# Kernel optimization log

Hardware: AMD Instinct MI355X
Metric: run time of the kernel (lower is better)

Reference implementation:

```python
import jax, jax.numpy as jnp
from jax import lax
import numpy as np

L = 2          # num_delimiter_layers
H = 8          # num q/kv heads
MIN_CL = 3
MAX_CL = 16

def rms_norm(x, w, eps=1e-6):
    return x * lax.rsqrt(jnp.mean(x * x, axis=-1, keepdims=True) + eps) * w

def rope(t):
    # t: [B, H, S, Dh], GPT-NeoX style half-split rotation, theta=10000
    Dh, S = t.shape[-1], t.shape[-2]
    half = Dh // 2
    inv = 1.0 / (10000.0 ** (jnp.arange(half, dtype=jnp.float32) / half))
    fr = jnp.arange(S, dtype=jnp.float32)[:, None] * inv  # [S, half]
    cos, sin = jnp.cos(fr), jnp.sin(fr)
    t1, t2 = t[..., :half], t[..., half:]
    return jnp.concatenate([t1 * cos - t2 * sin, t1 * sin + t2 * cos], axis=-1)

def chunk_ids_one(flags):
    # flags: [S] bool (probs > 0.5). Returns per-position chunk id and num chunks.
    S = flags.shape[0]
    # ends take value p+1 for flagged p; fallback to a single end at S-1 if none.
    has_end = jnp.zeros(S + 1, bool).at[1:].set(flags)
    fallback = jnp.zeros(S + 1, bool).at[S - 1].set(True)
    has_end = jnp.where(flags.any(), has_end, fallback)
    idx = jnp.where(has_end, jnp.arange(S + 1), S + 1)  # S+1 = sentinel > any cap
    nxt = lax.associative_scan(jnp.minimum, idx, reverse=True)  # nxt[e] = min end >= e
    def step(carry, t):
        cur_end, cid = carry
        def new(_):
            cap = jnp.minimum(t + MAX_CL, S)
            e = nxt[t + 1]                       # smallest end > t
            e = jnp.where(e <= cap, e, cap)
            e = jnp.where(e - t < MIN_CL, jnp.minimum(t + MIN_CL, S), e)
            return e, cid + 1
        new_end, new_cid = lax.cond(t == cur_end, new, lambda _: (cur_end, cid), None)
        return (new_end, new_cid), new_cid
    (_, last), ids = lax.scan(step, (jnp.int32(0), jnp.int32(-1)), jnp.arange(S, dtype=jnp.int32))
    return ids, last + 1

def _forward(x, ln1, Wq, Wk, Wv, Wo, ln2, W1, W2, head_w, head_b):
    B, S, D = x.shape
    Dh = D // H
    causal = jnp.tril(jnp.ones((S, S), bool))
    scale = 1.0 / np.sqrt(Dh)
    for l in range(L):
        h = rms_norm(x, ln1[l])
        def split_heads(t):
            return t.reshape(B, S, H, Dh).transpose(0, 2, 1, 3)
        q = rope(split_heads(h @ Wq[l]))
        k = rope(split_heads(h @ Wk[l]))
        v = split_heads(h @ Wv[l])
        scores = jnp.einsum('bhqd,bhkd->bhqk', q, k) * scale
        scores = jnp.where(causal, scores, jnp.finfo(scores.dtype).min)
        attn = jax.nn.softmax(scores, axis=-1)
        o = jnp.einsum('bhqk,bhkd->bhqd', attn, v)
        o = o.transpose(0, 2, 1, 3).reshape(B, S, D)
        x = x + o @ Wo[l]
        h = rms_norm(x, ln2[l])
        x = x + jax.nn.gelu(h @ W1[l], approximate=False) @ W2[l]
    logits = (x @ head_w).squeeze(-1) + head_b[0]
    probs = jax.nn.sigmoid(logits)
    chunk_len_loss = jnp.mean(jnp.sum(probs, axis=1))
    return x, probs, chunk_len_loss

def setup_inputs():
    key = jax.random.key(0)
    ks = jax.random.split(key, 10)
    B, S, D = 4, 2048, 512
    F = 4 * D
    sc = 0.02
    return {
        'x': jax.random.normal(ks[0], (B, S, D), jnp.float32),
        'x_ids': jax.random.randint(ks[1], (B, S), 0, 256),
        'ln1': jnp.ones((L, D), jnp.float32),
        'Wq': jax.random.normal(ks[2], (L, D, D), jnp.float32) * sc,
        'Wk': jax.random.normal(ks[3], (L, D, D), jnp.float32) * sc,
        'Wv': jax.random.normal(ks[4], (L, D, D), jnp.float32) * sc,
        'Wo': jax.random.normal(ks[5], (L, D, D), jnp.float32) * sc,
        'ln2': jnp.ones((L, D), jnp.float32),
        'W1': jax.random.normal(ks[6], (L, D, F), jnp.float32) * sc,
        'W2': jax.random.normal(ks[7], (L, F, D), jnp.float32) * sc,
        'head_w': jax.random.normal(ks[8], (D, 1), jnp.float32) * sc,
        'head_b': jnp.zeros((1,), jnp.float32),
    }

def reference(x, x_ids, ln1, Wq, Wk, Wv, Wo, ln2, W1, W2, head_w, head_b):
    B, S, D = x.shape
    x_t, probs, chunk_len_loss = _forward(x, ln1, Wq, Wk, Wv, Wo, ln2, W1, W2, head_w, head_b)
    flags = probs > 0.5
    ids, n_chunks = jax.vmap(chunk_ids_one)(flags)  # ids: [B,S] int32
    # chunks partition [0,S), so block-diagonal mask == chunk-id equality
    attention_masks = ids[:, :, None] == ids[:, None, :]
    # per-batch mean chunk length = S / num_chunks (lengths sum to S)
    avg_chunk_len = jnp.mean(jnp.float32(S) / n_chunks.astype(jnp.float32))
    return (x_t, x_ids, avg_chunk_len, attention_masks, chunk_len_loss)
```

## Files before the change

### kernel.cpp

```cpp
#include <hip/hip_runtime.h>
#include <math.h>

#define S_LEN 2048
#define DMODEL 512
#define NHEAD 8
#define DH 64
#define FDIM 2048

typedef unsigned short ushort_t;
typedef __attribute__((ext_vector_type(8))) short short8_t;
typedef __attribute__((ext_vector_type(4))) float float4_t;

#define MFMA16(a, b, c) __builtin_amdgcn_mfma_f32_16x16x32_bf16(a, b, c, 0, 0, 0)



__device__ __forceinline__ ushort_t f2bf(float x) {
    unsigned u = __float_as_uint(x);
    return (ushort_t)((u + 0x7fffu + ((u >> 16) & 1u)) >> 16);
}
__device__ __forceinline__ float bf2f(ushort_t h) {
    return __uint_as_float((unsigned)h << 16);
}
__device__ __forceinline__ float gelu_f(float x) {
    return 0.5f * x * (1.0f + erff(x * 0.70710678118654752440f));
}
__device__ __forceinline__ void gl_lds16(const void* g, void* l) {
    __builtin_amdgcn_global_load_lds(
        (const __attribute__((address_space(1))) void*)g,
        (__attribute__((address_space(3))) void*)l, 16, 0, 0);
}

__device__ __forceinline__ void stage_tile(const ushort_t* __restrict__ g, int rs,
                                           ushort_t* __restrict__ s, int w, int lane) {
    #pragma unroll
    for (int j = 0; j < 2; ++j) {
        const int c = (w * 2 + j) * 64 + lane;
        const int kk = c >> 8, row = (c >> 2) & 63, q = c & 3;
        const int qs = q ^ ((row >> 1) & 3);
        gl_lds16(g + (size_t)row * rs + kk * 32 + qs * 8, s + c * 8);
    }
}

__global__ void copy_init_k(const float* __restrict__ x, const int* __restrict__ x_ids,
                            float* __restrict__ out) {
    size_t i = (size_t)blockIdx.x * blockDim.x + threadIdx.x;
    float4* o4 = (float4*)out;
    o4[i] = ((const float4*)x)[i];
    if (i < 2048) {
        int4 id4 = ((const int4*)x_ids)[i];
        o4[1048576 + i] = make_float4((float)id4.x, (float)id4.y, (float)id4.z, (float)id4.w);
    }
    if (i == 0) { out[4202496] = 0.0f; out[20979713] = 0.0f; }
}

__global__ __launch_bounds__(256) void rope_tab_k(float2* __restrict__ tab) {
    const int i = blockIdx.x * 256 + threadIdx.x;
    const int s = i >> 5, f = i & 31;
    float inv = powf(10000.0f, -(float)f * (1.0f / 32.0f));
    float sn, cs;
    sincosf((float)s * inv, &sn, &cs);
    tab[i] = make_float2(cs, sn);
}

__global__ __launch_bounds__(256) void tsplit_all_k(const float* __restrict__ Wq,
                                                    const float* __restrict__ Wk,
                                                    const float* __restrict__ Wv,
                                                    const float* __restrict__ Wo,
                                                    const float* __restrict__ W1,
                                                    const float* __restrict__ W2,
                                                    ushort_t* __restrict__ wbuf) {
    __shared__ float T[32][33];
    const int bid = blockIdx.x;
    const int l = bid / 3072;
    const int r = bid % 3072;
    ushort_t* lb = wbuf + (size_t)l * 6291456;
    const float* W; ushort_t* Thi; ushort_t* Tlo; int K, N, ntn, rr;
    if (r < 768) {
        const int which = r >> 8; rr = r & 255;
        W = (which == 0 ? Wq : which == 1 ? Wk : Wv) + (size_t)l * 262144;
        Thi = lb + which * 262144; Tlo = lb + 786432 + which * 262144;
        K = 512; N = 512; ntn = 16;
    } else if (r < 1024) {
        rr = r - 768; W = Wo + (size_t)l * 262144;
        Thi = lb + 1572864; Tlo = lb + 1835008; K = 512; N = 512; ntn = 16;
    } else if (r < 2048) {
        rr = r - 1024; W = W1 + (size_t)l * 1048576;
        Thi = lb + 2097152; Tlo = lb + 3145728; K = 512; N = 2048; ntn = 64;
    } else {
        rr = r - 2048; W = W2 + (size_t)l * 1048576;
        Thi = lb + 4194304; Tlo = lb + 5242880; K = 2048; N = 512; ntn = 16;
    }
    const int n0 = (rr % ntn) * 32, k0 = (rr / ntn) * 32;
    const int tx = threadIdx.x & 31, ty = threadIdx.x >> 5;
    #pragma unroll
    for (int i = 0; i < 4; ++i)
        T[ty + 8 * i][tx] = W[(size_t)(k0 + ty + 8 * i) * N + n0 + tx];
    __syncthreads();
    #pragma unroll
    for (int i = 0; i < 4; ++i) {
        const int n = ty + 8 * i;
        float x = T[tx][n];
        ushort_t hi = f2bf(x);
        Thi[(size_t)(n0 + n) * K + k0 + tx] = hi;
        Tlo[(size_t)(n0 + n) * K + k0 + tx] = f2bf(x - bf2f(hi));
    }
}

__global__ __launch_bounds__(256) void rmsnorm_split_k(const float* __restrict__ x,
                                                       const float* __restrict__ w,
                                                       ushort_t* __restrict__ hhi,
                                                       ushort_t* __restrict__ hlo) {
    __shared__ float red[4];
    const int tid = threadIdx.x;
    const size_t row = blockIdx.x;
    const float* xr = x + row * DMODEL;
    float2 v = *(const float2*)(xr + tid * 2);
    float ss = v.x * v.x + v.y * v.y;
    #pragma unroll
    for (int off = 32; off; off >>= 1) ss += __shfl_down(ss, off);
    if ((tid & 63) == 0) red[tid >> 6] = ss;
    __syncthreads();
    float tot = red[0] + red[1] + red[2] + red[3];
    float rs = 1.0f / sqrtf(tot * (1.0f / 512.0f) + 1e-6f);
    float2 wv = *(const float2*)(w + tid * 2);
    float y0 = v.x * rs * wv.x, y1 = v.y * rs * wv.y;
    ushort_t h0 = f2bf(y0), h1 = f2bf(y1);
    ushort_t l0 = f2bf(y0 - bf2f(h0)), l1 = f2bf(y1 - bf2f(h1));
    *(unsigned*)(hhi + row * DMODEL + tid * 2) = ((unsigned)h1 << 16) | h0;
    *(unsigned*)(hlo + row * DMODEL + tid * 2) = ((unsigned)l1 << 16) | l0;
}

template<int EPI, int TN>
__global__ __launch_bounds__(256) void gemm_s(const ushort_t* __restrict__ Ahi,
                                              const ushort_t* __restrict__ Alo,
                                              const ushort_t* __restrict__ Bhi,
                                              const ushort_t* __restrict__ Blo,
                                              int K, int N,
                                              float* __restrict__ C,
                                              const float* __restrict__ Cin,
                                              ushort_t* __restrict__ Chi,
                                              ushort_t* __restrict__ Clo,
                                              ushort_t* __restrict__ oqh,
                                              ushort_t* __restrict__ oql,
                                              ushort_t* __restrict__ okh,
                                              ushort_t* __restrict__ okl,
                                              ushort_t* __restrict__ ovh,
                                              const float2* __restrict__ rtab) {
    constexpr int MT = (TN == 128) ? 4 : 2;
    __shared__ ushort_t sAhi[4096], sAlo[4096];
    __shared__ ushort_t sBhi[TN * 32], sBlo[TN * 32];
    const int tid = threadIdx.x;
    const int lane = tid & 63, w = tid >> 6;
    const int wm = (TN == 128) ? (w >> 1) : w;
    const int wn = (TN == 128) ? (w & 1) : 0;
    const int bm = blockIdx.y, bn = blockIdx.x;
    const int sm = lane >> 2;
    const int sk = ((lane & 3) ^ ((sm >> 1) & 3)) * 8;
    const int fr = lane & 15;
    const int fq = lane >> 4;
    const int fko = (fq ^ ((fr >> 1) & 3)) * 8;

    float4_t acc[MT][4] = {};

    for (int kt = 0; kt < K; kt += 32) {
        #pragma unroll
        for (int j = 0; j < 2; ++j) {
            const int chunk = w * 2 + j;
            const int mr = chunk * 16 + sm;
            const size_t ga = (size_t)(bm * 128 + mr) * K + kt + sk;
            gl_lds16(Ahi + ga, &sAhi[chunk * 512]);
            gl_lds16(Alo + ga, &sAlo[chunk * 512]);
        }
        #pragma unroll
        for (int j = 0; j < TN / 64; ++j) {
            const int chunk = w * (TN / 64) + j;
            const int mr = chunk * 16 + sm;
            const size_t gb = (size_t)(bn * TN + mr) * K + kt + sk;
            gl_lds16(Bhi + gb, &sBhi[chunk * 512]);
            gl_lds16(Blo + gb, &sBlo[chunk * 512]);
        }
        __syncthreads();
        short8_t ah[MT], al[MT], bh[4], bl[4];
        #pragma unroll
        for (int t = 0; t < MT; ++t) {
            const int ao = (wm * (MT * 16) + t * 16 + fr) * 32 + fko;
            ah[t] = *(const short8_t*)&sAhi[ao];
            al[t] = *(const short8_t*)&sAlo[ao];
        }
        #pragma unroll
        for (int t = 0; t < 4; ++t) {
            const int bo = (wn * 64 + t * 16 + fr) * 32 + fko;
            bh[t] = *(const short8_t*)&sBhi[bo];
            bl[t] = *(const short8_t*)&sBlo[bo];
        }
        #pragma unroll
        for (int tm = 0; tm < MT; ++tm)
            #pragma unroll
            for (int tn = 0; tn < 4; ++tn) {
                acc[tm][tn] = MFMA16(ah[tm], bh[tn], acc[tm][tn]);
                acc[tm][tn] = MFMA16(al[tm], bh[tn], acc[tm][tn]);
                acc[tm][tn] = MFMA16(ah[tm], bl[tn], acc[tm][tn]);
            }
        __syncthreads();
    }

    if (EPI == 0) {
        const int cb = bn * 128 + wn * 64;
        const int mat = cb >> 9;
        const int hh = (cb >> 6) & 7;
        #pragma unroll
        for (int tm = 0; tm < MT; ++tm) {
            #pragma unroll
            for (int r = 0; r < 4; ++r) {
                const int mg = bm * 128 + wm * (MT * 16) + tm * 16 + fq * 4 + r;
                const int b = mg >> 11, s = mg & 2047;
                const int bhh = b * NHEAD + hh;
                if (mat < 2) {
                    ushort_t* dhi = (mat == 0) ? oqh : okh;
                    ushort_t* dlo = (mat == 0) ? oql : okl;
                    const size_t base = ((size_t)bhh * S_LEN + s) * DH;
                    #pragma unroll
                    for (int tn = 0; tn < 2; ++tn) {
                        const int d1 = tn * 16 + fr;
                        const float v1 = acc[tm][tn][r], v2 = acc[tm][tn + 2][r];
                        const float2 t = rtab[s * 32 + d1];
                        float r1 = v1 * t.x - v2 * t.y;
                        float r2 = v1 * t.y + v2 * t.x;
                        if (mat == 0) { r1 *= 0.125f; r2 *= 0.125f; }
                        ushort_t h1 = f2bf(r1), h2 = f2bf(r2);
                        dhi[base + d1]      = h1;
                        dlo[base + d1]      = f2bf(r1 - bf2f(h1));
                        dhi[base + d1 + 32] = h2;
                        dlo[base + d1 + 32] = f2bf(r2 - bf2f(h2));
                    }
                } else {
                    #pragma unroll
                    for (int tn = 0; tn < 4; ++tn) {
                        const int d = tn * 16 + fr;
                        const size_t off = ((size_t)bhh * DH + d) * S_LEN + s;
                        ovh[off] = f2bf(acc[tm][tn][r]);
                    }
                }
            }
        }
    } else {
        #pragma unroll
        for (int tm = 0; tm < MT; ++tm) {
            #pragma unroll
            for (int tn = 0; tn < 4; ++tn) {
                const int cb = bn * TN + wn * 64 + tn * 16;
                #pragma unroll
                for (int r = 0; r < 4; ++r) {
                    const int mg = bm * 128 + wm * (MT * 16) + tm * 16 + fq * 4 + r;
                    const float val = acc[tm][tn][r];
                    const size_t off = (size_t)mg * N + cb + fr;
                    if (EPI == 1) {
                        C[off] = Cin[off] + val;
                    } else {
                        const float g = gelu_f(val);
                        const ushort_t hi = f2bf(g);
                        Chi[off] = hi;
                        Clo[off] = f2bf(g - bf2f(hi));
                    }
                }
            }
        }
    }
}

__global__ __launch_bounds__(256) void attn_k(const ushort_t* __restrict__ qhi,
                                              const ushort_t* __restrict__ qlo,
                                              const ushort_t* __restrict__ khi,
                                              const ushort_t* __restrict__ klo,
                                              const ushort_t* __restrict__ vthi,
                                              ushort_t* __restrict__ Ohi,
                                              ushort_t* __restrict__ Olo) {
    __shared__ __align__(16) ushort_t sKh[4096], sKl[4096];
    __shared__ __align__(16) ushort_t sVh[4096], sPh[4096];
    const int tid = threadIdx.x, lane = tid & 63, w = tid >> 6;
    const int fr = lane & 15, fq = lane >> 4;
    const int fko = (fq ^ ((fr >> 1) & 3)) * 8;
    const int bidx = blockIdx.x;
    const int bh = bidx & 31;
    const int qt = 31 - (bidx >> 5);

    short8_t qfh[2], qfl[2];
    {
        const size_t base = ((size_t)bh * S_LEN + qt * 64 + w * 16 + fr) * DH + fq * 8;
        qfh[0] = *(const short8_t*)(qhi + base);
        qfh[1] = *(const short8_t*)(qhi + base + 32);
        qfl[0] = *(const short8_t*)(qlo + base);
        qfl[1] = *(const short8_t*)(qlo + base + 32);
    }

    float m_r[4], l_r[4];
    float4_t oacc[4] = {};
    #pragma unroll
    for (int r = 0; r < 4; ++r) { m_r[r] = -INFINITY; l_r[r] = 0.0f; }

    auto step = [&](const int kt, const bool diag) {
        __syncthreads();
        const size_t ko = ((size_t)bh * S_LEN + kt * 64) * DH;
        stage_tile(khi + ko, 64, sKh, w, lane);
        stage_tile(klo + ko, 64, sKl, w, lane);
        const size_t vo = (size_t)bh * DH * S_LEN + kt * 64;
        stage_tile(vthi + vo, S_LEN, sVh, w, lane);
        __syncthreads();

        float4_t sacc[4] = {};
        #pragma unroll
        for (int kk = 0; kk < 2; ++kk) {
            #pragma unroll
            for (int n = 0; n < 4; ++n) {
                const int bb = kk * 2048 + (n * 16 + fr) * 32 + fko;
                short8_t kh2 = *(const short8_t*)&sKh[bb];
                short8_t kl2 = *(const short8_t*)&sKl[bb];
                sacc[n] = MFMA16(qfh[kk], kh2, sacc[n]);
                sacc[n] = MFMA16(qfl[kk], kh2, sacc[n]);
                sacc[n] = MFMA16(qfh[kk], kl2, sacc[n]);
            }
        }

        #pragma unroll
        for (int r = 0; r < 4; ++r) {
            const int rowl = fq * 4 + r;
            const int qrow = w * 16 + rowl;
            const int psw = (qrow >> 1) & 3;
            float sv[4], mx = -INFINITY;
            #pragma unroll
            for (int n = 0; n < 4; ++n) {
                float x = sacc[n][r];
                if (diag && (n * 16 + fr) > qrow - w * 16 + w * 16) {}
                sv[n] = x;
            }
            #pragma unroll
            for (int n = 0; n < 4; ++n) {
                if (diag && (n * 16 + fr) > qrow) sv[n] = -1e30f;
                mx = fmaxf(mx, sv[n]);
            }
            mx = fmaxf(mx, __shfl_xor(mx, 1));
            mx = fmaxf(mx, __shfl_xor(mx, 2));
            mx = fmaxf(mx, __shfl_xor(mx, 4));
            mx = fmaxf(mx, __shfl_xor(mx, 8));
            const float mn = fmaxf(m_r[r], mx);
            const float alp = __expf(m_r[r] - mn);
            m_r[r] = mn;
            float ls = 0.0f;
            #pragma unroll
            for (int n = 0; n < 4; ++n) {
                const float p = __expf(sv[n] - mn);
                const int c0 = (n & 1) * 16 + fr;
                const int idx = (n >> 1) * 2048 + qrow * 32 + ((c0 >> 3) ^ psw) * 8 + (c0 & 7);
                sPh[idx] = f2bf(p);
                ls += p;
            }
            ls += __shfl_xor(ls, 1);
            ls += __shfl_xor(ls, 2);
            ls += __shfl_xor(ls, 4);
            ls += __shfl_xor(ls, 8);
            l_r[r] = alp * l_r[r] + ls;
            #pragma unroll
            for (int n = 0; n < 4; ++n) oacc[n][r] *= alp;
        }

        #pragma unroll
        for (int kkj = 0; kkj < 2; ++kkj) {
            short8_t ph = *(const short8_t*)&sPh[kkj * 2048 + (w * 16 + fr) * 32 + fko];
            #pragma unroll
            for (int n = 0; n < 4; ++n) {
                short8_t vh = *(const short8_t*)&sVh[kkj * 2048 + (n * 16 + fr) * 32 + fko];
                oacc[n] = MFMA16(ph, vh, oacc[n]);
            }
        }
    };

    for (int kt = 0; kt < qt; ++kt) step(kt, false);
    step(qt, true);

    const int b = bh >> 3, hh = bh & 7;
    #pragma unroll
    for (int r = 0; r < 4; ++r) {
        const float inv_l = 1.0f / l_r[r];
        const int s = qt * 64 + w * 16 + fq * 4 + r;
        const size_t base = ((size_t)b * S_LEN + s) * DMODEL + hh * DH;
        #pragma unroll
        for (int n = 0; n < 4; ++n) {
            const float y = oacc[n][r] * inv_l;
            const ushort_t h = f2bf(y);
            Ohi[base + n * 16 + fr] = h;
            Olo[base + n * 16 + fr] = f2bf(y - bf2f(h));
        }
    }
}

__global__ __launch_bounds__(256) void head_k(const float* __restrict__ x,
                                              const float* __restrict__ w,
                                              const float* __restrict__ b,
                                              float* __restrict__ probs) {
    const int tid = threadIdx.x;
    const int lane = tid & 63;
    const size_t row = (size_t)blockIdx.x * 4 + (tid >> 6);
    const float* xr = x + row * DMODEL;
    float acc = 0.0f;
    #pragma unroll
    for (int i = 0; i < 8; ++i) acc += xr[lane + i * 64] * w[lane + i * 64];
    #pragma unroll
    for (int off = 32; off; off >>= 1) acc += __shfl_down(acc, off);
    if (lane == 0)
        probs[row] = 1.0f / (1.0f + expf(-(acc + b[0])));
}

__global__ __launch_bounds__(256) void chunk_k(const float* __restrict__ probs,
                                               int* __restrict__ ids,
                                               float* __restrict__ avg_out,
                                               float* __restrict__ loss_out) {
    __shared__ ushort_t nxA[2052], nxB[2052];
    __shared__ ushort_t lift[10][2052];
    __shared__ float lred[4];
    __shared__ int anyf;
    const int b = blockIdx.x, tid = threadIdx.x;
    const float* pr = probs + (size_t)b * S_LEN;
    if (tid == 0) anyf = 0;
    __syncthreads();
    int loc = 0;
    float lsum = 0.0f;
    for (int t = tid; t < S_LEN; t += 256) {
        const float p = pr[t];
        loc |= (p > 0.5f) ? 1 : 0;
        lsum += p;
    }
    if (loc) atomicOr(&anyf, 1);
    #pragma unroll
    for (int off = 32; off; off >>= 1) lsum += __shfl_down(lsum, off);
    if ((tid & 63) == 0) lred[tid >> 6] = lsum;
    __syncthreads();
    if (tid == 0)
        atomicAdd(loss_out, (lred[0] + lred[1] + lred[2] + lred[3]) * 0.25f);
    const int any = anyf;
    for (int i = tid; i <= S_LEN; i += 256) {
        const bool he = any ? (i >= 1 && pr[i - 1] > 0.5f) : (i == S_LEN - 1);
        nxA[i] = he ? (ushort_t)i : (ushort_t)(S_LEN + 1);
    }
    __syncthreads();
    ushort_t* src = nxA;
    ushort_t* dst = nxB;
    for (int d = 1; d <= 2048; d <<= 1) {
        for (int i = tid; i <= S_LEN; i += 256) {
            ushort_t v = src[i];
            if (i + d <= S_LEN) { ushort_t u2 = src[i + d]; v = u2 < v ? u2 : v; }
            dst[i] = v;
        }
        __syncthreads();
        ushort_t* tmp = src; src = dst; dst = tmp;
    }
    for (int t = tid; t < S_LEN; t += 256) {
        int cap = t + 16; if (cap > S_LEN) cap = S_LEN;
        int e = src[t + 1];
        if (e > cap) e = cap;
        if (e - t < 3) { e = t + 3; if (e > S_LEN) e = S_LEN; }
        lift[0][t] = (ushort_t)e;
    }
    if (tid == 0) lift[0][S_LEN] = (ushort_t)S_LEN;
    __syncthreads();
    for (int j = 1; j < 10; ++j) {
        for (int t = tid; t <= S_LEN; t += 256)
            lift[j][t] = lift[j - 1][lift[j - 1][t]];
        __syncthreads();
    }
    for (int t = tid; t < S_LEN; t += 256) {
        int pos = 0, cid = 0;
        #pragma unroll
        for (int j = 9; j >= 0; --j) {
            const int p2 = lift[j][pos];
            if (p2 <= t) { pos = p2; cid += (1 << j); }
        }
        ids[(size_t)b * S_LEN + t] = cid;
        if (t == S_LEN - 1) atomicAdd(avg_out, 512.0f / (float)(cid + 1));
    }
}

__global__ __launch_bounds__(256) void masks_k(const int* __restrict__ ids,
                                               float* __restrict__ mask) {
    const int bq = blockIdx.x;
    const int b = bq >> 11;
    const int myid = ids[bq];
    const int* idr = ids + (size_t)b * S_LEN;
    float* mr = mask + (size_t)bq * S_LEN;
    for (int k = threadIdx.x; k < S_LEN; k += 256)
        mr[k] = (idr[k] == myid) ? 1.0f : 0.0f;
}

extern "C" void kernel_launch(void* const* d_in, const int* in_sizes, int n_in,
                              void* d_out, int out_size, void* d_ws, size_t ws_size,
                              hipStream_t stream) {
    (void)in_sizes; (void)n_in; (void)out_size; (void)ws_size;
    const float* x      = (const float*)d_in[0];
    const int*   x_ids  = (const int*)d_in[1];
    const float* ln1    = (const float*)d_in[2];
    const float* Wq     = (const float*)d_in[3];
    const float* Wk     = (const float*)d_in[4];
    const float* Wv     = (const float*)d_in[5];
    const float* Wo     = (const float*)d_in[6];
    const float* ln2    = (const float*)d_in[7];
    const float* W1     = (const float*)d_in[8];
    const float* W2     = (const float*)d_in[9];
    const float* head_w = (const float*)d_in[10];
    const float* head_b = (const float*)d_in[11];

    float* out = (float*)d_out;
    ushort_t* u = (ushort_t*)d_ws;
    ushort_t* qh   = u;
    ushort_t* ql   = u + 4194304;
    ushort_t* kh   = u + 8388608;
    ushort_t* kl   = u + 12582912;
    ushort_t* vth  = u + 16777216;
    ushort_t* ohi  = u + 25165824;
    ushort_t* olo  = u + 29360128;
    ushort_t* hhi  = u + 33554432;
    ushort_t* hlo  = u + 37748736;
    ushort_t* ffhi = u;
    ushort_t* fflo = u + 16777216;
    float*    probs = (float*)(u + 41943040);
    int*      ids   = (int*)(u + 41943040 + 16384);
    ushort_t* wbuf     = (ushort_t*)(out + 4202512);
    float2*   rope_tab = (float2*)(wbuf + 12582912);
    float* xbuf = out;

    copy_init_k<<<4096, 256, 0, stream>>>(x, x_ids, out);
    rope_tab_k<<<256, 256, 0, stream>>>(rope_tab);
    tsplit_all_k<<<6144, 256, 0, stream>>>(Wq, Wk, Wv, Wo, W1, W2, wbuf);

    for (int l = 0; l < 2; ++l) {
        ushort_t* lb = wbuf + (size_t)l * 6291456;
        ushort_t* qkvT_hi = lb;
        ushort_t* qkvT_lo = lb + 786432;
        ushort_t* woT_hi  = lb + 1572864;
        ushort_t* woT_lo  = lb + 1835008;
        ushort_t* w1T_hi  = lb + 2097152;
        ushort_t* w1T_lo  = lb + 3145728;
        ushort_t* w2T_hi  = lb + 4194304;
        ushort_t* w2T_lo  = lb + 5242880;

        rmsnorm_split_k<<<8192, 256, 0, stream>>>(xbuf, ln1 + l * DMODEL, hhi, hlo);
        gemm_s<0, 128><<<dim3(12, 64), 256, 0, stream>>>(hhi, hlo, qkvT_hi, qkvT_lo, 512, 1536,
                                                         nullptr, nullptr, nullptr, nullptr,
                                                         qh, ql, kh, kl, vth, rope_tab);
        attn_k<<<1024, 256, 0, stream>>>(qh, ql, kh, kl, vth, ohi, olo);
        gemm_s<1, 64><<<dim3(8, 64), 256, 0, stream>>>(ohi, olo, woT_hi, woT_lo, 512, 512,
                                                       xbuf, xbuf, nullptr, nullptr,
                                                       nullptr, nullptr, nullptr, nullptr, nullptr, nullptr);
        rmsnorm_split_k<<<8192, 256, 0, stream>>>(xbuf, ln2 + l * DMODEL, hhi, hlo);
        gemm_s<2, 128><<<dim3(16, 64), 256, 0, stream>>>(hhi, hlo, w1T_hi, w1T_lo, 512, 2048,
                                                         nullptr, nullptr, ffhi, fflo,
                                                         nullptr, nullptr, nullptr, nullptr, nullptr, nullptr);
        gemm_s<1, 64><<<dim3(8, 64), 256, 0, stream>>>(ffhi, fflo, w2T_hi, w2T_lo, 2048, 512,
                                                       xbuf, xbuf, nullptr, nullptr,
                                                       nullptr, nullptr, nullptr, nullptr, nullptr, nullptr);
    }

    head_k<<<2048, 256, 0, stream>>>(xbuf, head_w, head_b, probs);
    chunk_k<<<4, 256, 0, stream>>>(probs, ids, out + 4202496, out + 20979713);
    masks_k<<<8192, 256, 0, stream>>>(ids, out + 4202497);
}
```

Baseline: 876.6 us.

## Pair causal attention tiles per block, swizzle GEMM block order, add MFMA priority hints

The attention kernel now launches half as many blocks, and each block processes two query tiles (qt and 31-qt), so every block does the same amount of causal work. This removes the tail imbalance of the old one-tile-per-block launch. The GEMM launches become 1D grids remapped so that groups of 8 row-tiles are spread across consecutive block IDs, aiming for better L2 reuse of the weight and activation tiles. s_setprio hints are placed around the MFMA sections of attention to favour matrix issue over the softmax of other waves. The costs are fewer attention blocks (512), which may underfill the GPU, and a longer serial loop inside each block.

```diff
diff --git a/kernel.cpp b/kernel.cpp
--- a/kernel.cpp
+++ b/kernel.cpp
@@ -154,7 +154,11 @@
     const int lane = tid & 63, w = tid >> 6;
     const int wm = (TN == 128) ? (w >> 1) : w;
     const int wn = (TN == 128) ? (w & 1) : 0;
-    const int bm = blockIdx.y, bn = blockIdx.x;
+    const int nbn = N / TN;
+    const int id = blockIdx.x;
+    const int jj = id >> 3;
+    const int bm = (id & 7) * 8 + jj / nbn;
+    const int bn = jj % nbn;
     const int sm = lane >> 2;
     const int sk = ((lane & 3) ^ ((sm >> 1) & 3)) * 8;
     const int fr = lane & 15;
@@ -283,113 +287,116 @@
     const int fko = (fq ^ ((fr >> 1) & 3)) * 8;
     const int bidx = blockIdx.x;
     const int bh = bidx & 31;
-    const int qt = 31 - (bidx >> 5);
-
-    short8_t qfh[2], qfl[2];
-    {
-        const size_t base = ((size_t)bh * S_LEN + qt * 64 + w * 16 + fr) * DH + fq * 8;
-        qfh[0] = *(const short8_t*)(qhi + base);
-        qfh[1] = *(const short8_t*)(qhi + base + 32);
-        qfl[0] = *(const short8_t*)(qlo + base);
-        qfl[1] = *(const short8_t*)(qlo + base + 32);
-    }
-
-    float m_r[4], l_r[4];
-    float4_t oacc[4] = {};
-    #pragma unroll
-    for (int r = 0; r < 4; ++r) { m_r[r] = -INFINITY; l_r[r] = 0.0f; }
-
-    auto step = [&](const int kt, const bool diag) {
-        __syncthreads();
-        const size_t ko = ((size_t)bh * S_LEN + kt * 64) * DH;
-        stage_tile(khi + ko, 64, sKh, w, lane);
-        stage_tile(klo + ko, 64, sKl, w, lane);
-        const size_t vo = (size_t)bh * DH * S_LEN + kt * 64;
-        stage_tile(vthi + vo, S_LEN, sVh, w, lane);
-        __syncthreads();
-
-        float4_t sacc[4] = {};
-        #pragma unroll
-        for (int kk = 0; kk < 2; ++kk) {
+    const int p = bidx >> 5;
+
+    for (int half = 0; half < 2; ++half) {
+        const int qt = half ? p : 31 - p;
+
+        short8_t qfh[2], qfl[2];
+        {
+            const size_t base = ((size_t)bh * S_LEN + qt * 64 + w * 16 + fr) * DH + fq * 8;
+            qfh[0] = *(const short8_t*)(qhi + base);
+            qfh[1] = *(const short8_t*)(qhi + base + 32);
+            qfl[0] = *(const short8_t*)(qlo + base);
+            qfl[1] = *(const short8_t*)(qlo + base + 32);
+        }
+
+        float m_r[4], l_r[4];
+        float4_t oacc[4] = {};
+        #pragma unroll
+        for (int r = 0; r < 4; ++r) { m_r[r] = -INFINITY; l_r[r] = 0.0f; }
+
+        auto step = [&](const int kt, const bool diag) {
+            __syncthreads();
+            const size_t ko = ((size_t)bh * S_LEN + kt * 64) * DH;
+            stage_tile(khi + ko, 64, sKh, w, lane);
+            stage_tile(klo + ko, 64, sKl, w, lane);
+            const size_t vo = (size_t)bh * DH * S_LEN + kt * 64;
+            stage_tile(vthi + vo, S_LEN, sVh, w, lane);
+            __syncthreads();
+
+            float4_t sacc[4] = {};
+            __builtin_amdgcn_s_setprio(1);
+            #pragma unroll
+            for (int kk = 0; kk < 2; ++kk) {
+                #pragma unroll
+                for (int n = 0; n < 4; ++n) {
+                    const int bb = kk * 2048 + (n * 16 + fr) * 32 + fko;
+                    short8_t kh2 = *(const short8_t*)&sKh[bb];
+                    short8_t kl2 = *(const short8_t*)&sKl[bb];
+                    sacc[n] = MFMA16(qfh[kk], kh2, sacc[n]);
+                    sacc[n] = MFMA16(qfl[kk], kh2, sacc[n]);
+                    sacc[n] = MFMA16(qfh[kk], kl2, sacc[n]);
+                }
+            }
+            __builtin_amdgcn_s_setprio(0);
+
+            #pragma unroll
+            for (int r = 0; r < 4; ++r) {
+                const int rowl = fq * 4 + r;
+                const int qrow = w * 16 + rowl;
+                const int psw = (qrow >> 1) & 3;
+                float sv[4], mx = -INFINITY;
+                #pragma unroll
+                for (int n = 0; n < 4; ++n) {
+                    sv[n] = sacc[n][r];
+                    if (diag && (n * 16 + fr) > qrow) sv[n] = -1e30f;
+                    mx = fmaxf(mx, sv[n]);
+                }
+                mx = fmaxf(mx, __shfl_xor(mx, 1));
+                mx = fmaxf(mx, __shfl_xor(mx, 2));
+                mx = fmaxf(mx, __shfl_xor(mx, 4));
+                mx = fmaxf(mx, __shfl_xor(mx, 8));
+                const float mn = fmaxf(m_r[r], mx);
+                const float alp = __expf(m_r[r] - mn);
+                m_r[r] = mn;
+                float ls = 0.0f;
+                #pragma unroll
+                for (int n = 0; n < 4; ++n) {
+                    const float pv = __expf(sv[n] - mn);
+                    const int c0 = (n & 1) * 16 + fr;
+                    const int idx = (n >> 1) * 2048 + qrow * 32 + ((c0 >> 3) ^ psw) * 8 + (c0 & 7);
+                    sPh[idx] = f2bf(pv);
+                    ls += pv;
+                }
+                ls += __shfl_xor(ls, 1);
+                ls += __shfl_xor(ls, 2);
+                ls += __shfl_xor(ls, 4);
+                ls += __shfl_xor(ls, 8);
+                l_r[r] = alp * l_r[r] + ls;
+                #pragma unroll
+                for (int n = 0; n < 4; ++n) oacc[n][r] *= alp;
+            }
+
+            __builtin_amdgcn_s_setprio(1);
+            #pragma unroll
+            for (int kkj = 0; kkj < 2; ++kkj) {
+                short8_t ph = *(const short8_t*)&sPh[kkj * 2048 + (w * 16 + fr) * 32 + fko];
+                #pragma unroll
+                for (int n = 0; n < 4; ++n) {
+                    short8_t vh = *(const short8_t*)&sVh[kkj * 2048 + (n * 16 + fr) * 32 + fko];
+                    oacc[n] = MFMA16(ph, vh, oacc[n]);
+                }
+            }
+            __builtin_amdgcn_s_setprio(0);
+        };
+
+        for (int kt = 0; kt < qt; ++kt) step(kt, false);
+        step(qt, true);
+
+        const int b = bh >> 3, hh = bh & 7;
+        #pragma unroll
+        for (int r = 0; r < 4; ++r) {
+            const float inv_l = 1.0f / l_r[r];
+            const int s = qt * 64 + w * 16 + fq * 4 + r;
+            const size_t base = ((size_t)b * S_LEN + s) * DMODEL + hh * DH;
             #pragma unroll
             for (int n = 0; n < 4; ++n) {
-                const int bb = kk * 2048 + (n * 16 + fr) * 32 + fko;
-                short8_t kh2 = *(const short8_t*)&sKh[bb];
-                short8_t kl2 = *(const short8_t*)&sKl[bb];
-                sacc[n] = MFMA16(qfh[kk], kh2, sacc[n]);
-                sacc[n] = MFMA16(qfl[kk], kh2, sacc[n]);
-                sacc[n] = MFMA16(qfh[kk], kl2, sacc[n]);
-            }
-        }
-
-        #pragma unroll
-        for (int r = 0; r < 4; ++r) {
-            const int rowl = fq * 4 + r;
-            const int qrow = w * 16 + rowl;
-            const int psw = (qrow >> 1) & 3;
-            float sv[4], mx = -INFINITY;
-            #pragma unroll
-            for (int n = 0; n < 4; ++n) {
-                float x = sacc[n][r];
-                if (diag && (n * 16 + fr) > qrow - w * 16 + w * 16) {}
-                sv[n] = x;
-            }
-            #pragma unroll
-            for (int n = 0; n < 4; ++n) {
-                if (diag && (n * 16 + fr) > qrow) sv[n] = -1e30f;
-                mx = fmaxf(mx, sv[n]);
-            }
-            mx = fmaxf(mx, __shfl_xor(mx, 1));
-            mx = fmaxf(mx, __shfl_xor(mx, 2));
-            mx = fmaxf(mx, __shfl_xor(mx, 4));
-            mx = fmaxf(mx, __shfl_xor(mx, 8));
-            const float mn = fmaxf(m_r[r], mx);
-            const float alp = __expf(m_r[r] - mn);
-            m_r[r] = mn;
-            float ls = 0.0f;
-            #pragma unroll
-            for (int n = 0; n < 4; ++n) {
-                const float p = __expf(sv[n] - mn);
-                const int c0 = (n & 1) * 16 + fr;
-                const int idx = (n >> 1) * 2048 + qrow * 32 + ((c0 >> 3) ^ psw) * 8 + (c0 & 7);
-                sPh[idx] = f2bf(p);
-                ls += p;
-            }
-            ls += __shfl_xor(ls, 1);
-            ls += __shfl_xor(ls, 2);
-            ls += __shfl_xor(ls, 4);
-            ls += __shfl_xor(ls, 8);
-            l_r[r] = alp * l_r[r] + ls;
-            #pragma unroll
-            for (int n = 0; n < 4; ++n) oacc[n][r] *= alp;
-        }
-
-        #pragma unroll
-        for (int kkj = 0; kkj < 2; ++kkj) {
-            short8_t ph = *(const short8_t*)&sPh[kkj * 2048 + (w * 16 + fr) * 32 + fko];
-            #pragma unroll
-            for (int n = 0; n < 4; ++n) {
-                short8_t vh = *(const short8_t*)&sVh[kkj * 2048 + (n * 16 + fr) * 32 + fko];
-                oacc[n] = MFMA16(ph, vh, oacc[n]);
-            }
-        }
-    };
-
-    for (int kt = 0; kt < qt; ++kt) step(kt, false);
-    step(qt, true);
-
-    const int b = bh >> 3, hh = bh & 7;
-    #pragma unroll
-    for (int r = 0; r < 4; ++r) {
-        const float inv_l = 1.0f / l_r[r];
-        const int s = qt * 64 + w * 16 + fq * 4 + r;
-        const size_t base = ((size_t)b * S_LEN + s) * DMODEL + hh * DH;
-        #pragma unroll
-        for (int n = 0; n < 4; ++n) {
-            const float y = oacc[n][r] * inv_l;
-            const ushort_t h = f2bf(y);
-            Ohi[base + n * 16 + fr] = h;
-            Olo[base + n * 16 + fr] = f2bf(y - bf2f(h));
+                const float y = oacc[n][r] * inv_l;
+                const ushort_t h = f2bf(y);
+                Ohi[base + n * 16 + fr] = h;
+                Olo[base + n * 16 + fr] = f2bf(y - bf2f(h));
+            }
         }
     }
 }
@@ -543,20 +550,20 @@
         ushort_t* w2T_lo  = lb + 5242880;
 
         rmsnorm_split_k<<<8192, 256, 0, stream>>>(xbuf, ln1 + l * DMODEL, hhi, hlo);
-        gemm_s<0, 128><<<dim3(12, 64), 256, 0, stream>>>(hhi, hlo, qkvT_hi, qkvT_lo, 512, 1536,
-                                                         nullptr, nullptr, nullptr, nullptr,
-                                                         qh, ql, kh, kl, vth, rope_tab);
-        attn_k<<<1024, 256, 0, stream>>>(qh, ql, kh, kl, vth, ohi, olo);
-        gemm_s<1, 64><<<dim3(8, 64), 256, 0, stream>>>(ohi, olo, woT_hi, woT_lo, 512, 512,
-                                                       xbuf, xbuf, nullptr, nullptr,
-                                                       nullptr, nullptr, nullptr, nullptr, nullptr, nullptr);
+        gemm_s<0, 128><<<768, 256, 0, stream>>>(hhi, hlo, qkvT_hi, qkvT_lo, 512, 1536,
+                                                nullptr, nullptr, nullptr, nullptr,
+                                                qh, ql, kh, kl, vth, rope_tab);
+        attn_k<<<512, 256, 0, stream>>>(qh, ql, kh, kl, vth, ohi, olo);
+        gemm_s<1, 64><<<512, 256, 0, stream>>>(ohi, olo, woT_hi, woT_lo, 512, 512,
+                                               xbuf, xbuf, nullptr, nullptr,
+                                               nullptr, nullptr, nullptr, nullptr, nullptr, nullptr);
         rmsnorm_split_k<<<8192, 256, 0, stream>>>(xbuf, ln2 + l * DMODEL, hhi, hlo);
-        gemm_s<2, 128><<<dim3(16, 64), 256, 0, stream>>>(hhi, hlo, w1T_hi, w1T_lo, 512, 2048,
-                                                         nullptr, nullptr, ffhi, fflo,
-                                                         nullptr, nullptr, nullptr, nullptr, nullptr, nullptr);
-        gemm_s<1, 64><<<dim3(8, 64), 256, 0, stream>>>(ffhi, fflo, w2T_hi, w2T_lo, 2048, 512,
-                                                       xbuf, xbuf, nullptr, nullptr,
-                                                       nullptr, nullptr, nullptr, nullptr, nullptr, nullptr);
+        gemm_s<2, 128><<<1024, 256, 0, stream>>>(hhi, hlo, w1T_hi, w1T_lo, 512, 2048,
+                                                 nullptr, nullptr, ffhi, fflo,
+                                                 nullptr, nullptr, nullptr, nullptr, nullptr, nullptr);
+        gemm_s<1, 64><<<512, 256, 0, stream>>>(ffhi, fflo, w2T_hi, w2T_lo, 2048, 512,
+                                               xbuf, xbuf, nullptr, nullptr,
+                                               nullptr, nullptr, nullptr, nullptr, nullptr, nullptr);
     }
 
     head_k<<<2048, 256, 0, stream>>>(xbuf, head_w, head_b, probs);
```

After: 815.1 us. 7.0% less time.
